# Kernel tuning notes

Hardware: AMD Instinct MI355X
Metric: run time of the kernel (lower is better)

## Reference

```python
import jax, jax.numpy as jnp
import numpy as np
import math

B, S, E = 2, 2048, 1024
H = 16
D = E // H  # head dim = 64


def setup_inputs() -> dict:
    key = jax.random.key(0)
    ks = jax.random.split(key, 9)
    s = 1.0 / math.sqrt(E)
    return {
        "x": jax.random.normal(ks[0], (B, S, E), dtype=jnp.float32),
        "Wq": jax.random.uniform(ks[1], (E, E), jnp.float32, -s, s),
        "bq": jnp.zeros((E,), jnp.float32),
        "Wk": jax.random.uniform(ks[2], (E, E), jnp.float32, -s, s),
        "bk": jnp.zeros((E,), jnp.float32),
        "Wv": jax.random.uniform(ks[3], (E, E), jnp.float32, -s, s),
        "bv": jnp.zeros((E,), jnp.float32),
        "Wo": jax.random.uniform(ks[4], (E, E), jnp.float32, -s, s),
        "bo": jnp.zeros((E,), jnp.float32),
    }


def reference(x, Wq, bq, Wk, bk, Wv, bv, Wo, bo):
    b, s, e = x.shape
    q = x @ Wq + bq  # [B,S,E]
    k = x @ Wk + bk
    v = x @ Wv + bv
    # [B,S,E] -> [B,H,S,D]
    q = q.reshape(b, s, H, D).transpose(0, 2, 1, 3)
    k = k.reshape(b, s, H, D).transpose(0, 2, 1, 3)
    v = v.reshape(b, s, H, D).transpose(0, 2, 1, 3)
    scores = jnp.einsum('bhqd,bhkd->bhqk', q, k) / jnp.sqrt(jnp.float32(D))
    causal = jnp.tril(jnp.ones((s, s), dtype=bool))  # keep lower triangle
    scores = jnp.where(causal, scores, -jnp.inf)
    attn = jax.nn.softmax(scores, axis=-1)
    # dropout is identity in eval mode
    out = jnp.einsum('bhqk,bhkd->bhqd', attn, v)
    out = out.transpose(0, 2, 1, 3).reshape(b, s, e)
    return out @ Wo + bo
```

## Files before the change

### kernel.cpp

```cpp
#include <hip/hip_runtime.h>
#include <hip/hip_bf16.h>
#include <math.h>

#define B_ 2
#define S_ 2048
#define E_ 1024
#define H_ 16
#define D_ 64
#define M_ (B_*S_)

typedef __attribute__((ext_vector_type(8))) short short8v;
typedef __attribute__((ext_vector_type(4))) float floatx4;

__device__ __forceinline__ short f2bf(float f) {
    union { float f; unsigned u; } x; x.f = f;
    unsigned r = (x.u + 0x7fffu + ((x.u >> 16) & 1u)) >> 16;
    return (short)r;
}

__device__ __forceinline__ unsigned pk_bf16(float a, float b) {
    union { float f; unsigned u; } x, y;
    x.f = a; y.f = b;
    return __builtin_amdgcn_perm(y.u + 0x8000u, x.u + 0x8000u, 0x07060302u);
}

__device__ __forceinline__ float fast_exp2(float x) {
#if __has_builtin(__builtin_amdgcn_exp2f)
    return __builtin_amdgcn_exp2f(x);
#else
    return __expf(x * 0.6931471805599453f);
#endif
}

__device__ __forceinline__ void gl2lds16(const void* g, void* l) {
    __builtin_amdgcn_global_load_lds(
        (const __attribute__((address_space(1))) void*)g,
        (__attribute__((address_space(3))) void*)l, 16, 0, 0);
}

__global__ __launch_bounds__(256) void convert_x(
    const float* __restrict__ x, short* __restrict__ xb)
{
    const size_t i = ((size_t)blockIdx.x*256 + threadIdx.x) * 8;
    float4 a = *(const float4*)(x + i);
    float4 b = *(const float4*)(x + i + 4);
    int4 p = { (int)pk_bf16(a.x,a.y), (int)pk_bf16(a.z,a.w),
               (int)pk_bf16(b.x,b.y), (int)pk_bf16(b.z,b.w) };
    *(int4*)(xb + i) = p;
}

__global__ __launch_bounds__(256) void transpose_w(
    const float* __restrict__ W0, const float* __restrict__ W1,
    const float* __restrict__ W2, const float* __restrict__ W3,
    short* __restrict__ T0, short* __restrict__ T1,
    short* __restrict__ T2, short* __restrict__ T3)
{
    const int z = blockIdx.z;
    const float* W = (z==0)?W0:(z==1)?W1:(z==2)?W2:W3;
    short*       T = (z==0)?T0:(z==1)?T1:(z==2)?T2:T3;
    __shared__ float tile[32][33];
    const int k0 = blockIdx.y*32, n0 = blockIdx.x*32;
    const int r = threadIdx.x >> 5, c = threadIdx.x & 31;
    #pragma unroll
    for (int i=0;i<4;i++)
        tile[r+8*i][c] = W[(size_t)(k0+r+8*i)*E_ + n0 + c];
    __syncthreads();
    #pragma unroll
    for (int i=0;i<4;i++)
        T[(size_t)(n0+r+8*i)*E_ + k0 + c] = f2bf(tile[c][r+8*i]);
}

__global__ __launch_bounds__(256) void qkv_gemm(
    const short* __restrict__ xb,
    const short* __restrict__ Wtq, const short* __restrict__ Wtk, const short* __restrict__ Wtv,
    const float* __restrict__ bq, const float* __restrict__ bk, const float* __restrict__ bv,
    short* __restrict__ Qo, short* __restrict__ Ko, short* __restrict__ Vo)
{
    const int z = blockIdx.z;
    const short* Wt = (z==0) ? Wtq : (z==1) ? Wtk : Wtv;
    const float* bb = (z==0) ? bq  : (z==1) ? bk  : bv;
    short* out      = (z==0) ? Qo  : (z==1) ? Ko  : Vo;
    const float sc  = (z==0) ? 0.18033688011112042f : 1.0f;

    __shared__ __align__(16) short As[128*32];
    __shared__ __align__(16) short Bs[128*32];

    const int t = threadIdx.x;
    const int wave = t >> 6, lane = t & 63;
    const int quad = lane >> 4, l15 = lane & 15;
    const int m0 = blockIdx.y*128, n0 = blockIdx.x*128;
    const int mq = (wave & 1)*64, nq = (wave >> 1)*64;
    const int srow = lane >> 2, scol = (lane & 3)*8;

    floatx4 acc[4][4];
    #pragma unroll
    for (int i=0;i<4;i++)
        #pragma unroll
        for (int j=0;j<4;j++) acc[i][j] = (floatx4){0.f,0.f,0.f,0.f};

    for (int k0 = 0; k0 < E_; k0 += 32) {
        #pragma unroll
        for (int p=0;p<2;p++) {
            const int rb = 16*(wave*2 + p);
            gl2lds16(xb + (size_t)(m0+rb+srow)*E_ + k0 + scol, &As[rb*32]);
            gl2lds16(Wt + (size_t)(n0+rb+srow)*E_ + k0 + scol, &Bs[rb*32]);
        }
        __syncthreads();
        short8v a[4], b[4];
        #pragma unroll
        for (int mt=0;mt<4;mt++) a[mt] = *(const short8v*)&As[(mq+mt*16+l15)*32 + quad*8];
        #pragma unroll
        for (int nt=0;nt<4;nt++) b[nt] = *(const short8v*)&Bs[(nq+nt*16+l15)*32 + quad*8];
        #pragma unroll
        for (int mt=0;mt<4;mt++)
            #pragma unroll
            for (int nt=0;nt<4;nt++)
                acc[mt][nt] = __builtin_amdgcn_mfma_f32_16x16x32_bf16(a[mt], b[nt], acc[mt][nt], 0,0,0);
        __syncthreads();
    }

    #pragma unroll
    for (int nt=0;nt<4;nt++) {
        const int n = n0 + nq + nt*16 + l15;
        const float bias = bb[n];
        const int h = n >> 6, d = n & 63;
        #pragma unroll
        for (int mt=0;mt<4;mt++) {
            #pragma unroll
            for (int r=0;r<4;r++) {
                const int m = m0 + mq + mt*16 + quad*4 + r;
                const int b2 = m >> 11, s = m & (S_-1);
                const float v = (acc[mt][nt][r] + bias) * sc;
                if (z == 2) out[((size_t)((b2<<4)+h)*D_ + d)*S_ + s] = f2bf(v);
                else        out[((size_t)((b2<<4)+h)*S_ + s)*D_ + d] = f2bf(v);
            }
        }
    }
}

__global__ __launch_bounds__(256, 1) void attn_kernel(
    const short* __restrict__ Q, const short* __restrict__ K, const short* __restrict__ V,
    short* __restrict__ AO)
{
    const int bh = blockIdx.x;
    const int qb = (gridDim.y - 1 - blockIdx.y) * 128;
    const int t = threadIdx.x;
    const int wave = t >> 6, lane = t & 63;
    const int quad = lane >> 4, l15 = lane & 15;

    const short* Qp = Q + (size_t)bh * (S_*D_);
    const short* Kp = K + (size_t)bh * (S_*D_);
    const short* Vp = V + (size_t)bh * (S_*D_);

    __shared__ __align__(16) short Psl[4*4*16*72];
    short* const pwav = Psl + wave*(4*16*72);
    short* const P0A = pwav;
    short* const P0B = pwav + 16*72;
    short* const P1A = pwav + 2*16*72;
    short* const P1B = pwav + 3*16*72;

    const int qA = qb + wave*16;
    const int qB = qb + 64 + wave*16;
    const short* qa = Qp + (size_t)(qA + l15)*D_ + quad*8;
    const short8v qA0 = *(const short8v*)qa, qA1 = *(const short8v*)(qa + 32);
    const short* qbp = Qp + (size_t)(qB + l15)*D_ + quad*8;
    const short8v qB0 = *(const short8v*)qbp, qB1 = *(const short8v*)(qbp + 32);

    const int qrbA = qA + quad*4;
    const int qrbB = qB + quad*4;

    floatx4 oA[4], oB[4];
    #pragma unroll
    for (int i=0;i<4;i++) { oA[i] = (floatx4){0,0,0,0}; oB[i] = (floatx4){0,0,0,0}; }
    float tsA[4] = {0,0,0,0}, tsB[4] = {0,0,0,0};

    const int L = (qb >> 6) + 2;

    auto load_k = [&](short8v (&kb)[4][2], int kt) {
        const int k0 = kt << 6;
        #pragma unroll
        for (int h=0; h<4; h++) {
            const short* kr = Kp + (size_t)(k0 + 4*l15 + h)*D_ + quad*8;
            kb[h][0] = *(const short8v*)kr;
            kb[h][1] = *(const short8v*)(kr + 32);
        }
    };
    auto load_v = [&](short8v (&vb)[4][2], int kt) {
        const int k0 = kt << 6;
        #pragma unroll
        for (int dt=0; dt<4; dt++) {
            const short* vr = Vp + (size_t)(dt*16 + l15)*S_ + k0 + quad*8;
            vb[dt][0] = *(const short8v*)vr;
            vb[dt][1] = *(const short8v*)(vr + 32);
        }
    };
    auto qk = [&](short8v (&kb)[4][2], const short8v& q0f, const short8v& q1f,
                  floatx4 (&s)[4]) {
        #pragma unroll
        for (int h=0; h<4; h++) {
            s[h] = (floatx4){0.f,0.f,0.f,0.f};
            s[h] = __builtin_amdgcn_mfma_f32_16x16x32_bf16(q0f, kb[h][0], s[h], 0,0,0);
            s[h] = __builtin_amdgcn_mfma_f32_16x16x32_bf16(q1f, kb[h][1], s[h], 0,0,0);
        }
    };
    auto soft_u = [&](floatx4 (&s)[4], float* ts, short* pw, int qrb, int k0) {
        const int kk = k0 + 4*l15;
        #pragma unroll
        for (int r=0; r<4; r++) {
            const int qr = qrb + r;
            float p[4];
            #pragma unroll
            for (int h=0; h<4; h++) {
                const float e = fast_exp2(s[h][r]);
                p[h] = (kk + h > qr) ? 0.f : e;
            }
            ts[r] += (p[0] + p[1]) + (p[2] + p[3]);
            int2 pkv = { (int)pk_bf16(p[0], p[1]), (int)pk_bf16(p[2], p[3]) };
            *(int2*)(pw + (quad*4 + r)*72 + l15*4) = pkv;
        }
    };
    auto pv = [&](short8v (&vb)[4][2], const short* pw, floatx4 (&o)[4]) {
        const short8v pf0 = *(const short8v*)(pw + l15*72 + quad*8);
        const short8v pf1 = *(const short8v*)(pw + l15*72 + 32 + quad*8);
        #pragma unroll
        for (int dt=0; dt<4; dt++) {
            o[dt] = __builtin_amdgcn_mfma_f32_16x16x32_bf16(pf0, vb[dt][0], o[dt], 0,0,0);
            o[dt] = __builtin_amdgcn_mfma_f32_16x16x32_bf16(pf1, vb[dt][1], o[dt], 0,0,0);
        }
    };

    short8v kX[4][2], kY[4][2], vX[4][2], vY[4][2];

    load_k(kX, 0);
    load_v(vX, 0);
    {
        floatx4 sA[4], sB[4];
        qk(kX, qA0, qA1, sA);
        qk(kX, qB0, qB1, sB);
        load_k(kY, 1);
        soft_u(sA, tsA, P0A, qrbA, 0);
        soft_u(sB, tsB, P0B, qrbB, 0);
        load_v(vY, 1);
    }

    int kt = 1;
    for (;;) {
        {
            floatx4 sA[4], sB[4];
            qk(kY, qA0, qA1, sA);
            qk(kY, qB0, qB1, sB);
            if (kt + 1 < L) load_k(kX, kt + 1);
            pv(vX, P0A, oA);
            pv(vX, P0B, oB);
            const int k0 = kt << 6;
            soft_u(sA, tsA, P1A, qrbA, k0);
            soft_u(sB, tsB, P1B, qrbB, k0);
            if (kt + 1 < L) load_v(vX, kt + 1);
        }
        kt++;
        if (kt >= L) break;
        {
            floatx4 sA[4], sB[4];
            qk(kX, qA0, qA1, sA);
            qk(kX, qB0, qB1, sB);
            if (kt + 1 < L) load_k(kY, kt + 1);
            pv(vY, P1A, oA);
            pv(vY, P1B, oB);
            const int k0 = kt << 6;
            soft_u(sA, tsA, P0A, qrbA, k0);
            soft_u(sB, tsB, P0B, qrbB, k0);
            if (kt + 1 < L) load_v(vY, kt + 1);
        }
        kt++;
    }

    pv(vY, P1A, oA);
    pv(vY, P1B, oB);

    float lA[4], lB[4];
    #pragma unroll
    for (int r=0; r<4; r++) {
        float a = tsA[r], b = tsB[r];
        #pragma unroll
        for (int off=1; off<16; off<<=1) {
            a += __shfl_xor(a, off);
            b += __shfl_xor(b, off);
        }
        lA[r] = a; lB[r] = b;
    }

    const int b = bh >> 4, h = bh & 15;
    #pragma unroll
    for (int dt=0; dt<4; dt++) {
        #pragma unroll
        for (int r=0; r<4; r++) {
            const int d = dt*16 + l15;
            const int sA_ = qA + quad*4 + r;
            const int sB_ = qB + quad*4 + r;
            AO[((size_t)(b*S_ + sA_)*H_ + h)*D_ + d] = f2bf(oA[dt][r] / lA[r]);
            AO[((size_t)(b*S_ + sB_)*H_ + h)*D_ + d] = f2bf(oB[dt][r] / lB[r]);
        }
    }
}

__global__ __launch_bounds__(256) void out_gemm(
    const short* __restrict__ A, const short* __restrict__ Wto,
    const float* __restrict__ bo, float* __restrict__ out)
{
    __shared__ __align__(16) short As[128*32];
    __shared__ __align__(16) short Bs[128*32];

    const int t = threadIdx.x;
    const int wave = t >> 6, lane = t & 63;
    const int quad = lane >> 4, l15 = lane & 15;
    const int m0 = blockIdx.y*128, n0 = blockIdx.x*128;
    const int mq = (wave & 1)*64, nq = (wave >> 1)*64;
    const int srow = lane >> 2, scol = (lane & 3)*8;

    floatx4 acc[4][4];
    #pragma unroll
    for (int i=0;i<4;i++)
        #pragma unroll
        for (int j=0;j<4;j++) acc[i][j] = (floatx4){0.f,0.f,0.f,0.f};

    for (int k0 = 0; k0 < E_; k0 += 32) {
        #pragma unroll
        for (int p=0;p<2;p++) {
            const int rb = 16*(wave*2 + p);
            gl2lds16(A   + (size_t)(m0+rb+srow)*E_ + k0 + scol, &As[rb*32]);
            gl2lds16(Wto + (size_t)(n0+rb+srow)*E_ + k0 + scol, &Bs[rb*32]);
        }
        __syncthreads();
        short8v a[4], b[4];
        #pragma unroll
        for (int mt=0;mt<4;mt++) a[mt] = *(const short8v*)&As[(mq+mt*16+l15)*32 + quad*8];
        #pragma unroll
        for (int nt=0;nt<4;nt++) b[nt] = *(const short8v*)&Bs[(nq+nt*16+l15)*32 + quad*8];
        #pragma unroll
        for (int mt=0;mt<4;mt++)
            #pragma unroll
            for (int nt=0;nt<4;nt++)
                acc[mt][nt] = __builtin_amdgcn_mfma_f32_16x16x32_bf16(a[mt], b[nt], acc[mt][nt], 0,0,0);
        __syncthreads();
    }

    #pragma unroll
    for (int nt=0;nt<4;nt++) {
        const int n = n0 + nq + nt*16 + l15;
        const float bias = bo[n];
        #pragma unroll
        for (int mt=0;mt<4;mt++) {
            #pragma unroll
            for (int r=0;r<4;r++) {
                const int m = m0 + mq + mt*16 + quad*4 + r;
                out[(size_t)m*E_ + n] = acc[mt][nt][r] + bias;
            }
        }
    }
}

extern "C" void kernel_launch(void* const* d_in, const int* in_sizes, int n_in,
                              void* d_out, int out_size, void* d_ws, size_t ws_size,
                              hipStream_t stream)
{
    const float* x  = (const float*)d_in[0];
    const float* Wq = (const float*)d_in[1];
    const float* bq = (const float*)d_in[2];
    const float* Wk = (const float*)d_in[3];
    const float* bk = (const float*)d_in[4];
    const float* Wv = (const float*)d_in[5];
    const float* bv = (const float*)d_in[6];
    const float* Wo = (const float*)d_in[7];
    const float* bo = (const float*)d_in[8];

    short* xb  = (short*)d_ws;
    short* Tq  = xb  + (size_t)M_ * E_;
    short* Tk  = Tq  + (size_t)E_ * E_;
    short* Tv  = Tk  + (size_t)E_ * E_;
    short* To  = Tv  + (size_t)E_ * E_;
    short* Qw  = To  + (size_t)E_ * E_;
    short* Kw  = Qw  + (size_t)M_ * E_;
    short* Vw  = Kw  + (size_t)M_ * E_;
    short* AOw = Vw  + (size_t)M_ * E_;

    dim3 blk(256);
    convert_x<<<dim3((M_*E_)/(256*8)), blk, 0, stream>>>(x, xb);
    transpose_w<<<dim3(E_/32, E_/32, 4), blk, 0, stream>>>(Wq, Wk, Wv, Wo, Tq, Tk, Tv, To);
    qkv_gemm<<<dim3(E_/128, M_/128, 3), blk, 0, stream>>>(xb, Tq, Tk, Tv, bq, bk, bv, Qw, Kw, Vw);
    attn_kernel<<<dim3(B_*H_, S_/128), blk, 0, stream>>>(Qw, Kw, Vw, AOw);
    out_gemm<<<dim3(E_/128, M_/128), blk, 0, stream>>>(AOw, To, bo, (float*)d_out);
}
```

Before: 218.3 us.

## Stage K/V tiles in shared LDS with swizzled layout and double buffering

```diff
diff --git a/kernel.cpp b/kernel.cpp
--- a/kernel.cpp
+++ b/kernel.cpp
@@ -130,9 +130,19 @@
             for (int r=0;r<4;r++) {
                 const int m = m0 + mq + mt*16 + quad*4 + r;
                 const int b2 = m >> 11, s = m & (S_-1);
+                const int bh = (b2<<4) + h;
                 const float v = (acc[mt][nt][r] + bias) * sc;
-                if (z == 2) out[((size_t)((b2<<4)+h)*D_ + d)*S_ + s] = f2bf(v);
-                else        out[((size_t)((b2<<4)+h)*S_ + s)*D_ + d] = f2bf(v);
+                if (z == 0) {
+                    out[((size_t)bh*S_ + s)*D_ + d] = f2bf(v);
+                } else if (z == 1) {
+                    const int ts = s >> 6, kk = s & 63;
+                    const int c = kk*8 + ((d>>3) ^ ((kk>>2)&7));
+                    out[((size_t)bh*32 + ts)*4096 + c*8 + (d&7)] = f2bf(v);
+                } else {
+                    const int ts = s >> 6, sk = s & 63;
+                    const int c = d*8 + ((sk>>3) ^ (d&7));
+                    out[((size_t)bh*32 + ts)*4096 + c*8 + (sk&7)] = f2bf(v);
+                }
             }
         }
     }
@@ -152,12 +162,8 @@
     const short* Kp = K + (size_t)bh * (S_*D_);
     const short* Vp = V + (size_t)bh * (S_*D_);
 
-    __shared__ __align__(16) short Psl[4*4*16*72];
-    short* const pwav = Psl + wave*(4*16*72);
-    short* const P0A = pwav;
-    short* const P0B = pwav + 16*72;
-    short* const P1A = pwav + 2*16*72;
-    short* const P1B = pwav + 3*16*72;
+    __shared__ __align__(16) short KVs[2][8192];
+    __shared__ __align__(16) short Psl[2][4][2][16*72];
 
     const int qA = qb + wave*16;
     const int qB = qb + 64 + wave*16;
@@ -176,31 +182,27 @@
 
     const int L = (qb >> 6) + 2;
 
-    auto load_k = [&](short8v (&kb)[4][2], int kt) {
-        const int k0 = kt << 6;
+    const int swz = l15 & 7;
+
+    auto stage = [&](int kt, int p) {
+        const short* src = ((wave < 2) ? Kp : Vp) + (size_t)kt*4096 + (wave&1)*2048 + lane*8;
+        short* dst = &KVs[p][((wave < 2) ? 0 : 4096) + (wave&1)*2048];
+        #pragma unroll
+        for (int c=0;c<4;c++)
+            gl2lds16(src + c*512, dst + c*512);
+    };
+    auto qk2 = [&](const short* KL, floatx4 (&sA)[4], floatx4 (&sB)[4]) {
         #pragma unroll
         for (int h=0; h<4; h++) {
-            const short* kr = Kp + (size_t)(k0 + 4*l15 + h)*D_ + quad*8;
-            kb[h][0] = *(const short8v*)kr;
-            kb[h][1] = *(const short8v*)(kr + 32);
-        }
-    };
-    auto load_v = [&](short8v (&vb)[4][2], int kt) {
-        const int k0 = kt << 6;
-        #pragma unroll
-        for (int dt=0; dt<4; dt++) {
-            const short* vr = Vp + (size_t)(dt*16 + l15)*S_ + k0 + quad*8;
-            vb[dt][0] = *(const short8v*)vr;
-            vb[dt][1] = *(const short8v*)(vr + 32);
-        }
-    };
-    auto qk = [&](short8v (&kb)[4][2], const short8v& q0f, const short8v& q1f,
-                  floatx4 (&s)[4]) {
-        #pragma unroll
-        for (int h=0; h<4; h++) {
-            s[h] = (floatx4){0.f,0.f,0.f,0.f};
-            s[h] = __builtin_amdgcn_mfma_f32_16x16x32_bf16(q0f, kb[h][0], s[h], 0,0,0);
-            s[h] = __builtin_amdgcn_mfma_f32_16x16x32_bf16(q1f, kb[h][1], s[h], 0,0,0);
+            const int rowc = (4*l15 + h)*8;
+            short8v b0 = *(const short8v*)(KL + (rowc + (quad       ^ swz))*8);
+            short8v b1 = *(const short8v*)(KL + (rowc + ((4 + quad) ^ swz))*8);
+            sA[h] = (floatx4){0.f,0.f,0.f,0.f};
+            sA[h] = __builtin_amdgcn_mfma_f32_16x16x32_bf16(qA0, b0, sA[h], 0,0,0);
+            sA[h] = __builtin_amdgcn_mfma_f32_16x16x32_bf16(qA1, b1, sA[h], 0,0,0);
+            sB[h] = (floatx4){0.f,0.f,0.f,0.f};
+            sB[h] = __builtin_amdgcn_mfma_f32_16x16x32_bf16(qB0, b0, sB[h], 0,0,0);
+            sB[h] = __builtin_amdgcn_mfma_f32_16x16x32_bf16(qB1, b1, sB[h], 0,0,0);
         }
     };
     auto soft_u = [&](floatx4 (&s)[4], float* ts, short* pw, int qrb, int k0) {
@@ -219,63 +221,54 @@
             *(int2*)(pw + (quad*4 + r)*72 + l15*4) = pkv;
         }
     };
-    auto pv = [&](short8v (&vb)[4][2], const short* pw, floatx4 (&o)[4]) {
+    short8v vr[4][2];
+    auto loadv = [&](const short* VL) {
+        #pragma unroll
+        for (int dt=0; dt<4; dt++) {
+            const int rowc = (dt*16 + l15)*8;
+            vr[dt][0] = *(const short8v*)(VL + (rowc + (quad       ^ swz))*8);
+            vr[dt][1] = *(const short8v*)(VL + (rowc + ((4 + quad) ^ swz))*8);
+        }
+    };
+    auto pv = [&](const short* pw, floatx4 (&o)[4]) {
         const short8v pf0 = *(const short8v*)(pw + l15*72 + quad*8);
         const short8v pf1 = *(const short8v*)(pw + l15*72 + 32 + quad*8);
         #pragma unroll
         for (int dt=0; dt<4; dt++) {
-            o[dt] = __builtin_amdgcn_mfma_f32_16x16x32_bf16(pf0, vb[dt][0], o[dt], 0,0,0);
-            o[dt] = __builtin_amdgcn_mfma_f32_16x16x32_bf16(pf1, vb[dt][1], o[dt], 0,0,0);
-        }
-    };
-
-    short8v kX[4][2], kY[4][2], vX[4][2], vY[4][2];
-
-    load_k(kX, 0);
-    load_v(vX, 0);
+            o[dt] = __builtin_amdgcn_mfma_f32_16x16x32_bf16(pf0, vr[dt][0], o[dt], 0,0,0);
+            o[dt] = __builtin_amdgcn_mfma_f32_16x16x32_bf16(pf1, vr[dt][1], o[dt], 0,0,0);
+        }
+    };
+
+    stage(0, 0);
+    __syncthreads();
+    stage(1, 1);
     {
+        const short* KL = &KVs[0][0];
         floatx4 sA[4], sB[4];
-        qk(kX, qA0, qA1, sA);
-        qk(kX, qB0, qB1, sB);
-        load_k(kY, 1);
-        soft_u(sA, tsA, P0A, qrbA, 0);
-        soft_u(sB, tsB, P0B, qrbB, 0);
-        load_v(vY, 1);
-    }
-
-    int kt = 1;
-    for (;;) {
-        {
-            floatx4 sA[4], sB[4];
-            qk(kY, qA0, qA1, sA);
-            qk(kY, qB0, qB1, sB);
-            if (kt + 1 < L) load_k(kX, kt + 1);
-            pv(vX, P0A, oA);
-            pv(vX, P0B, oB);
-            const int k0 = kt << 6;
-            soft_u(sA, tsA, P1A, qrbA, k0);
-            soft_u(sB, tsB, P1B, qrbB, k0);
-            if (kt + 1 < L) load_v(vX, kt + 1);
-        }
-        kt++;
-        if (kt >= L) break;
-        {
-            floatx4 sA[4], sB[4];
-            qk(kX, qA0, qA1, sA);
-            qk(kX, qB0, qB1, sB);
-            if (kt + 1 < L) load_k(kY, kt + 1);
-            pv(vY, P1A, oA);
-            pv(vY, P1B, oB);
-            const int k0 = kt << 6;
-            soft_u(sA, tsA, P0A, qrbA, k0);
-            soft_u(sB, tsB, P0B, qrbB, k0);
-            if (kt + 1 < L) load_v(vY, kt + 1);
-        }
-        kt++;
-    }
-
-    pv(vY, P1A, oA);
-    pv(vY, P1B, oB);
+        qk2(KL, sA, sB);
+        loadv(&KVs[0][4096]);
+        soft_u(sA, tsA, &Psl[0][wave][0][0], qrbA, 0);
+        soft_u(sB, tsB, &Psl[0][wave][1][0], qrbB, 0);
+    }
+
+    for (int kt = 1; kt < L; kt++) {
+        const int p = kt & 1;
+        __syncthreads();
+        if (kt + 1 < L) stage(kt + 1, p ^ 1);
+        const short* KL = &KVs[p][0];
+        floatx4 sA[4], sB[4];
+        qk2(KL, sA, sB);
+        pv(&Psl[p^1][wave][0][0], oA);
+        pv(&Psl[p^1][wave][1][0], oB);
+        loadv(&KVs[p][4096]);
+        const int k0 = kt << 6;
+        soft_u(sA, tsA, &Psl[p][wave][0][0], qrbA, k0);
+        soft_u(sB, tsB, &Psl[p][wave][1][0], qrbB, k0);
+    }
+
+    pv(&Psl[1][wave][0][0], oA);
+    pv(&Psl[1][wave][1][0], oB);
 
     float lA[4], lB[4];
     #pragma unroll
```

New measurement: 206.1 us. -5.6%, faster.
